# Kernel optimization log

Measured on AMD Instinct MI355X. Metric: run time of the kernel, lower is better.

## Reference

```python
import jax, jax.numpy as jnp
from jax import lax
import numpy as np

# db3 analysis/synthesis filter bank (pywt coefficients)
DEC_LO = np.array([0.035226291882100656, -0.085441273882241486, -0.13501102001039084,
                   0.45987750211933132, 0.80689150931333875, 0.33267055295095688], dtype=np.float32)
DEC_HI = np.array([-0.33267055295095688, 0.80689150931333875, -0.45987750211933132,
                   -0.13501102001039084, 0.085441273882241486, 0.035226291882100656], dtype=np.float32)
REC_LO = DEC_LO[::-1].copy()
REC_HI = np.array([0.035226291882100656, 0.085441273882241486, -0.13501102001039084,
                   -0.45987750211933132, 0.80689150931333875, -0.33267055295095688], dtype=np.float32)
L = 6  # db3 filter length
DN = ('NCHW', 'OIHW', 'NCHW')

# analysis correlation kernels (torch conv2d correlates, pytorch_wavelets pre-flips dec filters)
H0_A = jnp.asarray(DEC_LO[::-1].copy())
H1_A = jnp.asarray(DEC_HI[::-1].copy())
# synthesis: conv_transpose(x, g, stride=2, pad=L-2) == correlate(dilate(x,2), flip(g), pad=1)
G0_S = jnp.asarray(REC_LO[::-1].copy())
G1_S = jnp.asarray(REC_HI[::-1].copy())


def _sep_conv(x, f, axis, stride=1, lhs_dil=1, pad=0):
    """Depthwise 1-D correlation along H (axis=2) or W (axis=3) of an NCHW tensor."""
    C = x.shape[1]
    if axis == 2:
        k = jnp.tile(f.reshape(1, 1, -1, 1), (C, 1, 1, 1))
        strides, dil, padding = (stride, 1), (lhs_dil, 1), ((pad, pad), (0, 0))
    else:
        k = jnp.tile(f.reshape(1, 1, 1, -1), (C, 1, 1, 1))
        strides, dil, padding = (1, stride), (1, lhs_dil), ((0, 0), (pad, pad))
    return lax.conv_general_dilated(x, k, strides, padding, lhs_dilation=dil,
                                    dimension_numbers=DN, feature_group_count=C)


def _dwt2(x):
    # single-level separable 2D DWT, mode='zero' (pytorch_wavelets: rows then cols)
    lo = _sep_conv(x, H0_A, 3, stride=2, pad=L - 2)
    hi = _sep_conv(x, H1_A, 3, stride=2, pad=L - 2)
    ll = _sep_conv(lo, H0_A, 2, stride=2, pad=L - 2)
    lh = _sep_conv(lo, H1_A, 2, stride=2, pad=L - 2)  # yh[:,:,0]
    hl = _sep_conv(hi, H0_A, 2, stride=2, pad=L - 2)  # yh[:,:,1]
    hh = _sep_conv(hi, H1_A, 2, stride=2, pad=L - 2)  # yh[:,:,2]
    return ll, lh, hl, hh


def _idwt2(ll, lh, hl, hh):
    # inverse: cols then rows; transposed conv realized as lhs_dilation=2 + pad 1
    lo = _sep_conv(ll, G0_S, 2, lhs_dil=2, pad=1) + _sep_conv(lh, G1_S, 2, lhs_dil=2, pad=1)
    hi = _sep_conv(hl, G0_S, 2, lhs_dil=2, pad=1) + _sep_conv(hh, G1_S, 2, lhs_dil=2, pad=1)
    return _sep_conv(lo, G0_S, 3, lhs_dil=2, pad=1) + _sep_conv(hi, G1_S, 3, lhs_dil=2, pad=1)


def _dw3x3(x, w):
    # depthwise 3x3, padding 1, no bias; w: (C,1,3,3)
    return lax.conv_general_dilated(x, w, (1, 1), ((1, 1), (1, 1)),
                                    dimension_numbers=DN, feature_group_count=x.shape[1])


def _ssl(x, conv5_w, conv7_w, conv9_w):
    # faithful to original: conv5 applied to BOTH yl and ylh; conv1/conv_cat unused
    ll, lh, hl, hh = _dwt2(x)
    return _idwt2(_dw3x3(ll, conv5_w), _dw3x3(lh, conv5_w),
                  _dw3x3(hl, conv7_w), _dw3x3(hh, conv9_w))


def setup_inputs() -> dict:
    key = jax.random.key(0)
    ks = jax.random.split(key, 7)
    B, C, H, W, HEADS = 4, 256, 192, 192, 8
    s = 0.05
    return {
        'x': jax.random.normal(ks[0], (B, C, H, W), jnp.float32),
        'qkv_w': jax.random.normal(ks[1], (2 * C, C), jnp.float32) * s,        # 1x1 conv C->2C
        'qkv_conv_w': jax.random.normal(ks[2], (2 * C, 1, 3, 3), jnp.float32) * s,  # depthwise 3x3
        'conv5_w': jax.random.normal(ks[3], (C, 1, 3, 3), jnp.float32) * s,
        'conv7_w': jax.random.normal(ks[4], (C, 1, 3, 3), jnp.float32) * s,
        'conv9_w': jax.random.normal(ks[5], (C, 1, 3, 3), jnp.float32) * s,
        'proj_w': jax.random.normal(ks[6], (C, C), jnp.float32) * s,           # 1x1 conv C->C
        'temperature': jnp.ones((1, HEADS, 1, 1), jnp.float32),
        'num_heads': HEADS,
    }


def reference(x, qkv_w, qkv_conv_w, conv5_w, conv7_w, conv9_w, proj_w, temperature, num_heads):
    b, c, h, w = x.shape
    eps = 1e-12
    kv = jnp.einsum('oc,bchw->bohw', qkv_w, x)          # 1x1 conv, no bias
    kv = _dw3x3(kv, qkv_conv_w)
    k, v = jnp.split(kv, 2, axis=1)
    q = _ssl(x, conv5_w, conv7_w, conv9_w)              # wavelet query path, same HxW
    d = c // num_heads
    q = q.reshape(b, num_heads, d, h * w)
    k = k.reshape(b, num_heads, d, h * w)
    v = v.reshape(b, num_heads, d, h * w)
    q = q / jnp.maximum(jnp.linalg.norm(q, axis=-1, keepdims=True), eps)
    k = k / jnp.maximum(jnp.linalg.norm(k, axis=-1, keepdims=True), eps)
    attn = jax.nn.softmax(jnp.einsum('bhdn,bhen->bhde', q, k) * temperature, axis=-1)  # (b,H,d,d)
    out = jnp.einsum('bhde,bhen->bhdn', attn, v).reshape(b, c, h, w)
    return jnp.einsum('oc,bchw->bohw', proj_w, out)
```

## Files before the change

### kernel.cpp

```cpp
#include <hip/hip_runtime.h>
#include <hip/hip_bf16.h>

typedef __hip_bfloat16 bf16;
typedef __attribute__((ext_vector_type(8))) short short8v;
typedef __attribute__((ext_vector_type(4))) float f32x4;

#define NB 4
#define NC 256
#define NPIX 36864
#define NH 192
#define NW 192
#define SW 98
#define SH 98
#define GCH 24

__device__ __constant__ float cH0A[6] = {  0.33267055295095688f,  0.80689150931333875f,  0.45987750211933132f, -0.13501102001039084f, -0.085441273882241486f, 0.035226291882100656f };
__device__ __constant__ float cH1A[6] = {  0.035226291882100656f, 0.085441273882241486f, -0.13501102001039084f, -0.45987750211933132f,  0.80689150931333875f, -0.33267055295095688f };
__device__ __constant__ float cG0S[6] = {  0.035226291882100656f, -0.085441273882241486f, -0.13501102001039084f, 0.45987750211933132f,  0.80689150931333875f,  0.33267055295095688f };
__device__ __constant__ float cG1S[6] = { -0.33267055295095688f,  0.80689150931333875f, -0.45987750211933132f, -0.13501102001039084f,  0.085441273882241486f, 0.035226291882100656f };

__device__ inline unsigned short bfbits(float f) {
    bf16 h = __float2bfloat16(f);
    return *reinterpret_cast<unsigned short*>(&h);
}
__device__ inline float b2f(short s) {
    return __bfloat162float(*reinterpret_cast<const bf16*>(&s));
}

__global__ __launch_bounds__(256) void k_wave(const float* __restrict__ x,
                                              const float* __restrict__ w5, const float* __restrict__ w7,
                                              const float* __restrict__ w9,
                                              bf16* __restrict__ q, float* __restrict__ qsum) {
    int w0 = blockIdx.x * 64, h0 = blockIdx.y * 32;
    int bc = blockIdx.z;
    int c = bc & 255;
    int jh0 = h0 >> 1, jw0 = w0 >> 1;
    int xr0 = h0 - 6;
    int xc0 = w0 - 8;
    __shared__ __align__(16) char smem[40320];
    float (*s_x)[80]   = (float(*)[80])smem;
    float (*s_c)[36]   = (float(*)[36])smem;
    float (*s_lo)[40]  = (float(*)[40])(smem + 14080);
    float (*s_hi)[40]  = (float(*)[40])(smem + 21120);
    float (*s_lh)[36]  = (float(*)[36])(smem + 14080);
    float (*s_sub)[38] = (float(*)[38])(smem + 28160);
    __shared__ float s_w[4][9];
    __shared__ float red[4];
    const float* xp = x + (size_t)bc * NPIX;
    int t = threadIdx.x;
    if (t < 36) {
        int f = t / 9, k = t - f * 9;
        const float* wsel = (f <= 1) ? w5 : (f == 2 ? w7 : w9);
        s_w[f][k] = wsel[c * 9 + k];
    }
    for (int e = t; e < 880; e += 256) {
        int r = e / 20, s = e - r * 20;
        int row = xr0 + r, col0 = xc0 + s * 4;
        float4 v = make_float4(0.f, 0.f, 0.f, 0.f);
        if (row >= 0 && row < NH) {
            if (col0 >= 0 && col0 + 3 < NW) {
                v = *reinterpret_cast<const float4*>(xp + (size_t)row * NW + col0);
            } else {
#pragma unroll
                for (int j = 0; j < 4; ++j) {
                    int cc = col0 + j;
                    if (cc >= 0 && cc < NW) (&v.x)[j] = xp[(size_t)row * NW + cc];
                }
            }
        }
        *reinterpret_cast<float4*>(&s_x[r][s * 4]) = v;
    }
    __syncthreads();
    for (int e = t; e < 836; e += 256) {
        int r = e / 19, g = e - r * 19;
        float v[8];
#pragma unroll
        for (int j = 0; j < 8; ++j) v[j] = s_x[r][4 * g + j];
        float la0 = 0.f, ha0 = 0.f, la1 = 0.f, ha1 = 0.f;
#pragma unroll
        for (int tp = 0; tp < 6; ++tp) {
            la0 = fmaf(v[tp], cH0A[tp], la0);
            ha0 = fmaf(v[tp], cH1A[tp], ha0);
            la1 = fmaf(v[tp + 2], cH0A[tp], la1);
            ha1 = fmaf(v[tp + 2], cH1A[tp], ha1);
        }
        s_lo[r][2 * g] = la0;     s_hi[r][2 * g] = ha0;
        s_lo[r][2 * g + 1] = la1; s_hi[r][2 * g + 1] = ha1;
    }
    __syncthreads();
    for (int e = t; e < 760; e += 256) {
        int r = e / 38, jc = e - r * 38;
        int gr = jh0 - 1 + r, gcol = jw0 - 2 + jc;
        bool inb = (gr >= 0 && gr < SH && gcol >= 0 && gcol < SW);
        float ll = 0.f, lh = 0.f, hl = 0.f, hh = 0.f;
#pragma unroll
        for (int tp = 0; tp < 6; ++tp) {
            float lv = s_lo[2 * r + tp][jc];
            float hv = s_hi[2 * r + tp][jc];
            ll = fmaf(lv, cH0A[tp], ll); lh = fmaf(lv, cH1A[tp], lh);
            hl = fmaf(hv, cH0A[tp], hl); hh = fmaf(hv, cH1A[tp], hh);
        }
        s_sub[r][jc]      = inb ? ll : 0.f;
        s_sub[20 + r][jc] = inb ? lh : 0.f;
        s_sub[40 + r][jc] = inb ? hl : 0.f;
        s_sub[60 + r][jc] = inb ? hh : 0.f;
    }
    __syncthreads();
    for (int e = t; e < 612; e += 256) {
        int pl = e / 153;
        int r2 = e - pl * 153;
        int rp = r2 / 17, gp4 = r2 - rp * 17;
        const float* wp = s_w[pl];
        int rb = pl * 20 + 2 * rp;
        int cc = 2 * gp4;
        float win[4][4];
#pragma unroll
        for (int ri = 0; ri < 4; ++ri)
#pragma unroll
            for (int cj = 0; cj < 4; ++cj)
                win[ri][cj] = s_sub[rb + ri][cc + 1 + cj];
        float wreg[9];
#pragma unroll
        for (int i = 0; i < 9; ++i) wreg[i] = wp[i];
#pragma unroll
        for (int dr = 0; dr < 2; ++dr)
#pragma unroll
            for (int dc = 0; dc < 2; ++dc) {
                float a = 0.f;
#pragma unroll
                for (int ky = 0; ky < 3; ++ky)
#pragma unroll
                    for (int kx = 0; kx < 3; ++kx)
                        a = fmaf(win[dr + ky][dc + kx], wreg[ky * 3 + kx], a);
                s_c[pl * 18 + 2 * rp + dr][cc + dc] = a;
            }
    }
    __syncthreads();
    for (int e = t; e < 1088; e += 256) {
        int row = e / 34, cc = e - row * 34;
        int which = row >> 4, m = row & 15;
        float c0_0 = s_c[which * 36 + m][cc],     c1_0 = s_c[which * 36 + 18 + m][cc];
        float c0_1 = s_c[which * 36 + m + 1][cc], c1_1 = s_c[which * 36 + 18 + m + 1][cc];
        float c0_2 = s_c[which * 36 + m + 2][cc], c1_2 = s_c[which * 36 + 18 + m + 2][cc];
        float ae = c0_0 * cG0S[1] + c0_1 * cG0S[3] + c0_2 * cG0S[5]
                 + c1_0 * cG1S[1] + c1_1 * cG1S[3] + c1_2 * cG1S[5];
        float ao = c0_0 * cG0S[0] + c0_1 * cG0S[2] + c0_2 * cG0S[4]
                 + c1_0 * cG1S[0] + c1_1 * cG1S[2] + c1_2 * cG1S[4];
        s_lh[which * 32 + 2 * m][cc] = ae;
        s_lh[which * 32 + 2 * m + 1][cc] = ao;
    }
    __syncthreads();
    float lsum = 0.f;
    bf16* qp = q + (size_t)bc * NPIX;
#pragma unroll
    for (int it = 0; it < 4; ++it) {
        int e = t + 256 * it;
        int hh = e >> 5, m = e & 31;
        float l0 = s_lh[hh][m],     h0v = s_lh[32 + hh][m];
        float l1 = s_lh[hh][m + 1], h1v = s_lh[32 + hh][m + 1];
        float l2 = s_lh[hh][m + 2], h2v = s_lh[32 + hh][m + 2];
        float ae = l0 * cG0S[1] + l1 * cG0S[3] + l2 * cG0S[5]
                 + h0v * cG1S[1] + h1v * cG1S[3] + h2v * cG1S[5];
        float ao = l0 * cG0S[0] + l1 * cG0S[2] + l2 * cG0S[4]
                 + h0v * cG1S[0] + h1v * cG1S[2] + h2v * cG1S[4];
        unsigned pack = (unsigned)bfbits(ae) | ((unsigned)bfbits(ao) << 16);
        *reinterpret_cast<unsigned*>(qp + (size_t)(h0 + hh) * NW + w0 + 2 * m) = pack;
        lsum = fmaf(ae, ae, lsum);
        lsum = fmaf(ao, ao, lsum);
    }
#pragma unroll
    for (int off = 32; off; off >>= 1) lsum += __shfl_down(lsum, off, 64);
    if ((t & 63) == 0) red[t >> 6] = lsum;
    __syncthreads();
    if (t == 0) atomicAdd(&qsum[bc], red[0] + red[1] + red[2] + red[3]);
}

__global__ __launch_bounds__(256) void k_cvtw(const float* __restrict__ w, bf16* __restrict__ wb) {
    int idx = blockIdx.x * 256 + threadIdx.x;
    if (idx < 512 * 256) wb[idx] = __float2bfloat16(w[idx]);
}

__global__ __launch_bounds__(512) void k_gemm_x(const float* __restrict__ x, const bf16* __restrict__ Wbf,
                                                bf16* __restrict__ Out) {
    __shared__ __align__(16) short As[256 * 64];
    __shared__ __align__(16) short Bs[128 * 64];
    int nt = blockIdx.x, b = blockIdx.y;
    int n0 = nt * 128;
    const float* xb = x + (size_t)b * NC * NPIX;
    int t = threadIdx.x;
    int wv = t >> 6, l = t & 63;
    int wo = wv >> 1, wn = wv & 1;
    int lrow = l >> 3, cbs0 = l & 7;
    int nq = t & 31;
    int cg = t >> 5;
    int c0 = cg * 4;
    f32x4 z4 = {0.f, 0.f, 0.f, 0.f};
    f32x4 acc[4][4];
#pragma unroll
    for (int m = 0; m < 4; ++m)
#pragma unroll
        for (int nf = 0; nf < 4; ++nf) acc[m][nf] = z4;
    for (int kc = 0; kc < 256; kc += 64) {
        __syncthreads();
#pragma unroll
        for (int i = 0; i < 4; ++i) {
            int r0 = wv * 32 + i * 8;
            int r = r0 + lrow;
            int cb = cbs0 ^ (r & 7);
            __builtin_amdgcn_global_load_lds(
                (const __attribute__((address_space(1))) void*)(Wbf + (size_t)r * NC + kc + cb * 8),
                (__attribute__((address_space(3))) void*)(As + r0 * 64), 16, 0, 0);
        }
        float4 xv[4];
#pragma unroll
        for (int ci = 0; ci < 4; ++ci)
            xv[ci] = *reinterpret_cast<const float4*>(xb + (size_t)(kc + c0 + ci) * NPIX + n0 + nq * 4);
#pragma unroll
        for (int j = 0; j < 4; ++j) {
            int n = nq * 4 + j;
            ushort4 u;
            u.x = bfbits((&xv[0].x)[j]); u.y = bfbits((&xv[1].x)[j]);
            u.z = bfbits((&xv[2].x)[j]); u.w = bfbits((&xv[3].x)[j]);
            int unit = (c0 >> 3) ^ (n & 7);
            int half = (c0 >> 2) & 1;
            *reinterpret_cast<ushort4*>(Bs + n * 64 + unit * 8 + half * 4) = u;
        }
        __syncthreads();
#pragma unroll
        for (int kk = 0; kk < 2; ++kk) {
            int col8 = kk * 4 + (l >> 4);
            short8v av[4], bv[4];
#pragma unroll
            for (int m = 0; m < 4; ++m) {
                int row = wo * 64 + m * 16 + (l & 15);
                av[m] = *(const short8v*)(As + row * 64 + (col8 ^ (row & 7)) * 8);
            }
#pragma unroll
            for (int nf = 0; nf < 4; ++nf) {
                int row = wn * 64 + nf * 16 + (l & 15);
                bv[nf] = *(const short8v*)(Bs + row * 64 + (col8 ^ (row & 7)) * 8);
            }
#pragma unroll
            for (int m = 0; m < 4; ++m)
#pragma unroll
                for (int nf = 0; nf < 4; ++nf)
                    acc[m][nf] = __builtin_amdgcn_mfma_f32_16x16x32_bf16(av[m], bv[nf], acc[m][nf], 0, 0, 0);
        }
    }
    bf16* ob = Out + (size_t)b * NC * NPIX;
#pragma unroll
    for (int m = 0; m < 4; ++m)
#pragma unroll
        for (int nf = 0; nf < 4; ++nf)
#pragma unroll
            for (int r = 0; r < 4; ++r) {
                int oo = wo * 64 + m * 16 + (l >> 4) * 4 + r;
                int nn = n0 + wn * 64 + nf * 16 + (l & 15);
                ob[(size_t)oo * NPIX + nn] = __float2bfloat16(acc[m][nf][r]);
            }
}

template <typename TOUT>
__global__ __launch_bounds__(256) void k_gemm_bf(const bf16* __restrict__ X, const bf16* __restrict__ Wm,
                                                 int wStride, TOUT* __restrict__ Out) {
    __shared__ __align__(16) short As[128 * 64];
    __shared__ __align__(16) short Bs[128 * 64];
    int nt = blockIdx.x, ot = blockIdx.y, b = blockIdx.z;
    int n0 = nt * 128, o0 = ot * 128;
    const bf16* xb = X + (size_t)b * NPIX * NC;
    const bf16* Wb = Wm + (size_t)b * wStride;
    int t = threadIdx.x;
    int wv = t >> 6, l = t & 63;
    int wr = wv >> 1, wc = wv & 1;
    int lrow = l >> 3, cbs0 = l & 7;
    f32x4 z4 = {0.f, 0.f, 0.f, 0.f};
    f32x4 acc[4][4];
#pragma unroll
    for (int m = 0; m < 4; ++m)
#pragma unroll
        for (int nf = 0; nf < 4; ++nf) acc[m][nf] = z4;
    for (int kc = 0; kc < 256; kc += 64) {
        __syncthreads();
#pragma unroll
        for (int i = 0; i < 4; ++i) {
            int r0 = wv * 32 + i * 8;
            int r = r0 + lrow;
            int cb = cbs0 ^ (r & 7);
            __builtin_amdgcn_global_load_lds(
                (const __attribute__((address_space(1))) void*)(Wb + (size_t)(o0 + r) * NC + kc + cb * 8),
                (__attribute__((address_space(3))) void*)(As + r0 * 64), 16, 0, 0);
            __builtin_amdgcn_global_load_lds(
                (const __attribute__((address_space(1))) void*)(xb + (size_t)(n0 + r) * NC + kc + cb * 8),
                (__attribute__((address_space(3))) void*)(Bs + r0 * 64), 16, 0, 0);
        }
        __syncthreads();
#pragma unroll
        for (int kk = 0; kk < 2; ++kk) {
            int col8 = kk * 4 + (l >> 4);
            short8v av[4], bv[4];
#pragma unroll
            for (int m = 0; m < 4; ++m) {
                int row = wr * 64 + m * 16 + (l & 15);
                av[m] = *(const short8v*)(As + row * 64 + (col8 ^ (row & 7)) * 8);
            }
#pragma unroll
            for (int nf = 0; nf < 4; ++nf) {
                int row = wc * 64 + nf * 16 + (l & 15);
                bv[nf] = *(const short8v*)(Bs + row * 64 + (col8 ^ (row & 7)) * 8);
            }
#pragma unroll
            for (int m = 0; m < 4; ++m)
#pragma unroll
                for (int nf = 0; nf < 4; ++nf)
                    acc[m][nf] = __builtin_amdgcn_mfma_f32_16x16x32_bf16(av[m], bv[nf], acc[m][nf], 0, 0, 0);
        }
    }
    TOUT* ob = Out + (size_t)b * NC * NPIX;
#pragma unroll
    for (int m = 0; m < 4; ++m)
#pragma unroll
        for (int nf = 0; nf < 4; ++nf)
#pragma unroll
            for (int r = 0; r < 4; ++r) {
                int oo = o0 + wr * 64 + m * 16 + (l >> 4) * 4 + r;
                int nn = n0 + wc * 64 + nf * 16 + (l & 15);
                if constexpr (sizeof(TOUT) == 2)
                    ob[(size_t)oo * NPIX + nn] = __float2bfloat16(acc[m][nf][r]);
                else
                    ob[(size_t)oo * NPIX + nn] = acc[m][nf][r];
            }
}

__device__ inline short8v dw8(const bf16* __restrict__ chan, int r, int cb,
                              const float* __restrict__ w, float& ks) {
    float v[3][10];
#pragma unroll
    for (int ri = 0; ri < 3; ++ri) {
        int r2 = r + ri - 1;
        if (r2 < 0 || r2 >= NH) {
#pragma unroll
            for (int j = 0; j < 10; ++j) v[ri][j] = 0.f;
        } else {
            const bf16* p = chan + (size_t)r2 * NW + cb;
            short8v m = *(const short8v*)p;
            v[ri][0] = (cb > 0) ? __bfloat162float(p[-1]) : 0.f;
#pragma unroll
            for (int j = 0; j < 8; ++j) v[ri][j + 1] = b2f(m[j]);
            v[ri][9] = (cb < 184) ? __bfloat162float(p[8]) : 0.f;
        }
    }
    short8v out;
#pragma unroll
    for (int j = 0; j < 8; ++j) {
        float a = 0.f;
#pragma unroll
        for (int ri = 0; ri < 3; ++ri) {
            a = fmaf(v[ri][j],     w[ri * 3 + 0], a);
            a = fmaf(v[ri][j + 1], w[ri * 3 + 1], a);
            a = fmaf(v[ri][j + 2], w[ri * 3 + 2], a);
        }
        ks = fmaf(a, a, ks);
        out[j] = (short)bfbits(a);
    }
    return out;
}

__global__ __launch_bounds__(256) void k_gram_dw(const bf16* __restrict__ qbf, const bf16* __restrict__ kraw,
                                                 const float* __restrict__ dwW,
                                                 float* __restrict__ gpart, float* __restrict__ ksum) {
    int chunk = blockIdx.x;
    int bh = blockIdx.y; int b = bh >> 3, h = bh & 7;
    const bf16* qb = qbf + ((size_t)b * NC + h * 32) * NPIX;
    const bf16* kb = kraw + ((size_t)b * NC + h * 32) * NPIX;
    __shared__ float sg[4][1024];
    __shared__ float ksh[32];
    int t = threadIdx.x;
    int wv = t >> 6, l = t & 63;
    int dlo = l & 15, kslot = l >> 4;
    float wA[9], wB[9];
#pragma unroll
    for (int i = 0; i < 9; ++i) {
        wA[i] = dwW[(h * 32 + dlo) * 9 + i];
        wB[i] = dwW[(h * 32 + dlo + 16) * 9 + i];
    }
    const bf16* q0 = qb + (size_t)dlo * NPIX;
    const bf16* q1 = qb + (size_t)(dlo + 16) * NPIX;
    const bf16* k0 = kb + (size_t)dlo * NPIX;
    const bf16* k1 = kb + (size_t)(dlo + 16) * NPIX;
    f32x4 z4 = {0.f, 0.f, 0.f, 0.f};
    f32x4 a00 = z4, a01 = z4, a10 = z4, a11 = z4;
    float ks0 = 0.f, ks1 = 0.f;
    int r0 = chunk * 8 + wv * 2;
#pragma unroll
    for (int rr = 0; rr < 2; ++rr) {
        int r = r0 + rr;
#pragma unroll
        for (int c0 = 0; c0 < 192; c0 += 32) {
            int cb = c0 + kslot * 8;
            short8v av0 = *(const short8v*)(q0 + (size_t)r * NW + cb);
            short8v av1 = *(const short8v*)(q1 + (size_t)r * NW + cb);
            short8v bv0 = dw8(k0, r, cb, wA, ks0);
            short8v bv1 = dw8(k1, r, cb, wB, ks1);
            a00 = __builtin_amdgcn_mfma_f32_16x16x32_bf16(av0, bv0, a00, 0, 0, 0);
            a01 = __builtin_amdgcn_mfma_f32_16x16x32_bf16(av0, bv1, a01, 0, 0, 0);
            a10 = __builtin_amdgcn_mfma_f32_16x16x32_bf16(av1, bv0, a10, 0, 0, 0);
            a11 = __builtin_amdgcn_mfma_f32_16x16x32_bf16(av1, bv1, a11, 0, 0, 0);
        }
    }
    if (t < 32) ksh[t] = 0.f;
#pragma unroll
    for (int j = 0; j < 4; ++j) {
        int dA = kslot * 4 + j, dB = 16 + kslot * 4 + j;
        sg[wv][dA * 32 + dlo]      = a00[j];
        sg[wv][dA * 32 + 16 + dlo] = a01[j];
        sg[wv][dB * 32 + dlo]      = a10[j];
        sg[wv][dB * 32 + 16 + dlo] = a11[j];
    }
    __syncthreads();
    float* gp = gpart + ((size_t)bh * GCH + chunk) * 1024;
#pragma unroll
    for (int i = 0; i < 4; ++i) {
        int e = t + 256 * i;
        gp[e] = sg[0][e] + sg[1][e] + sg[2][e] + sg[3][e];
    }
    atomicAdd(&ksh[dlo], ks0);
    atomicAdd(&ksh[dlo + 16], ks1);
    __syncthreads();
    if (t < 32) atomicAdd(&ksum[b * NC + h * 32 + t], ksh[t]);
}

__global__ __launch_bounds__(1024) void k_attn(const float* __restrict__ gpart, const float* __restrict__ qsum,
                                               const float* __restrict__ ksum, const float* __restrict__ temp,
                                               float* __restrict__ attn) {
    int bh = blockIdx.x;
    int b = bh >> 3, h = bh & 7;
    int t = threadIdx.x;
    int d = t >> 5, e = t & 31;
    float s = 0.f;
    for (int i = 0; i < GCH; ++i) s += gpart[((size_t)bh * GCH + i) * 1024 + t];
    float rq = 1.f / fmaxf(sqrtf(qsum[b * NC + h * 32 + d]), 1e-12f);
    float rk = 1.f / fmaxf(sqrtf(ksum[b * NC + h * 32 + e]), 1e-12f);
    s *= rq * rk * temp[h];
    float m = s;
#pragma unroll
    for (int off = 16; off; off >>= 1) m = fmaxf(m, __shfl_xor(m, off, 32));
    float ex = expf(s - m);
    float sum = ex;
#pragma unroll
    for (int off = 16; off; off >>= 1) sum += __shfl_xor(sum, off, 32);
    attn[(size_t)bh * 1024 + t] = ex / sum;
}

__global__ __launch_bounds__(256) void k_wfold(const float* __restrict__ proj, const float* __restrict__ attn,
                                               bf16* __restrict__ wfbf) {
    int o = blockIdx.x, b = blockIdx.y;
    int t = threadIdx.x;
    int h = t >> 5, e = t & 31;
    const float* ap = attn + (size_t)(b * 8 + h) * 1024 + e;
    const float* pp = proj + o * NC + h * 32;
    float acc = 0.f;
#pragma unroll
    for (int d = 0; d < 32; ++d) acc = fmaf(pp[d], ap[d * 32], acc);
    wfbf[((size_t)b * NC + o) * NC + t] = __float2bfloat16(acc);
}

__global__ __launch_bounds__(256) void k_dwv(const bf16* __restrict__ vraw, const float* __restrict__ dwW,
                                             bf16* __restrict__ v2T) {
    int r = blockIdx.x;
    int cg = blockIdx.y;
    int b = blockIdx.z;
    __shared__ short s_v[3][32][204];
    const bf16* vb = vraw + ((size_t)b * NC + cg * 32) * NPIX;
    int t = threadIdx.x;
    for (int idx = t; idx < 4800; idx += 256) {
        int ri = idx / 1600;
        int rem = idx - ri * 1600;
        int e = rem / 50, j = rem - e * 50;
        int gr = r + ri - 1;
        int gc0 = -4 + 4 * j;
        ushort4 u = make_ushort4(0, 0, 0, 0);
        if (gr >= 0 && gr < NH && gc0 >= 0 && gc0 + 3 < NW)
            u = *reinterpret_cast<const ushort4*>(vb + (size_t)e * NPIX + (size_t)gr * NW + gc0);
        *reinterpret_cast<ushort4*>(&s_v[ri][e][4 * j]) = u;
    }
    int e = t & 31;
    int wslot = t >> 5;
    float w9[9];
#pragma unroll
    for (int i = 0; i < 9; ++i) w9[i] = dwW[(256 + cg * 32 + e) * 9 + i];
    __syncthreads();
    bf16* ob = v2T + ((size_t)b * NPIX + (size_t)r * NW) * NC + cg * 32 + e;
#pragma unroll
    for (int wi = 0; wi < 24; ++wi) {
        int w = wslot + 8 * wi;
        int cbase = w + 3;
        float a = 0.f;
#pragma unroll
        for (int ri = 0; ri < 3; ++ri) {
            a = fmaf(b2f(s_v[ri][e][cbase]),     w9[ri * 3 + 0], a);
            a = fmaf(b2f(s_v[ri][e][cbase + 1]), w9[ri * 3 + 1], a);
            a = fmaf(b2f(s_v[ri][e][cbase + 2]), w9[ri * 3 + 2], a);
        }
        ob[(size_t)w * NC] = __float2bfloat16(a);
    }
}


extern "C" void kernel_launch(void* const* d_in, const int* in_sizes, int n_in,
                              void* d_out, int out_size, void* d_ws, size_t ws_size,
                              hipStream_t stream) {
    (void)in_sizes; (void)n_in; (void)out_size;
    const float* x      = (const float*)d_in[0];
    const float* qkv_w  = (const float*)d_in[1];
    const float* qkv_cw = (const float*)d_in[2];
    const float* w5     = (const float*)d_in[3];
    const float* w7     = (const float*)d_in[4];
    const float* w9     = (const float*)d_in[5];
    const float* projw  = (const float*)d_in[6];
    const float* temp   = (const float*)d_in[7];

    const size_t OFF_SM    = 78675968;
    const size_t OFF_WBF   = OFF_SM;
    const size_t OFF_QSUM  = OFF_SM + 262144;
    const size_t OFF_KSUM  = OFF_QSUM + 4096;
    const size_t OFF_GPART = OFF_KSUM + 4096;
    const size_t OFF_ATTN  = OFF_GPART + 3145728;
    const size_t OFF_WF    = OFF_ATTN + 131072;
    const size_t WS_NEED   = OFF_WF + 524288;
    if (ws_size < WS_NEED) return;

    char* ws = (char*)d_ws;
    bf16*  kraw  = (bf16*)ws;
    bf16*  v2T   = (bf16*)ws;
    bf16*  wbf   = (bf16*)(ws + OFF_WBF);
    float* qsum  = (float*)(ws + OFF_QSUM);
    float* ksum  = (float*)(ws + OFF_KSUM);
    float* gpart = (float*)(ws + OFF_GPART);
    float* attn  = (float*)(ws + OFF_ATTN);
    bf16*  wfbf  = (bf16*)(ws + OFF_WF);

    bf16*  qbf  = (bf16*)((char*)d_out + 75497472);
    bf16*  vraw = (bf16*)((char*)d_out + 75497472);
    float* out  = (float*)d_out;

    hipMemsetAsync(ws + OFF_QSUM, 0, 8192, stream);

    k_wave<<<dim3(3, 6, NB * NC), 256, 0, stream>>>(x, w5, w7, w9, qbf, qsum);

    k_cvtw<<<512, 256, 0, stream>>>(qkv_w, wbf);

    k_gemm_x<<<dim3(288, NB), 512, 0, stream>>>(x, wbf, kraw);
    k_gram_dw<<<dim3(GCH, 32), 256, 0, stream>>>(qbf, kraw, qkv_cw, gpart, ksum);

    k_attn<<<32, 1024, 0, stream>>>(gpart, qsum, ksum, temp, attn);
    k_wfold<<<dim3(256, NB), 256, 0, stream>>>(projw, attn, wfbf);

    k_gemm_x<<<dim3(288, NB), 512, 0, stream>>>(x, wbf + 256 * 256, vraw);
    k_dwv<<<dim3(NH, 8, NB), 256, 0, stream>>>(vraw, qkv_cw, v2T);
    k_gemm_bf<float><<<dim3(288, 2, NB), 256, 0, stream>>>(v2T, wfbf, 65536, out);
}
```

Measured before the change: 520.1 us.

## Fuse K and V projection GEMMs to share one pass over x

Merges the two separate 1x1-conv GEMM launches for K and V into one kernel. It loads and converts each fp32 x tile to bf16 once, then runs MFMA against both weight halves, reloading only the weight tile in LDS between them. This removes a second full read and conversion of the large fp32 input. The cost is a doubled accumulator register footprint and extra barriers per K-chunk. V output is relocated to the start of the output buffer so it does not overlap q. The wavelet kernel's LDS reads and writes are also vectorized to float4/float2.

```diff
diff --git a/kernel.cpp b/kernel.cpp
--- a/kernel.cpp
+++ b/kernel.cpp
@@ -73,9 +73,9 @@
     __syncthreads();
     for (int e = t; e < 836; e += 256) {
         int r = e / 19, g = e - r * 19;
-        float v[8];
-#pragma unroll
-        for (int j = 0; j < 8; ++j) v[j] = s_x[r][4 * g + j];
+        float4 va = *reinterpret_cast<const float4*>(&s_x[r][4 * g]);
+        float4 vb = *reinterpret_cast<const float4*>(&s_x[r][4 * g + 4]);
+        float v[8] = { va.x, va.y, va.z, va.w, vb.x, vb.y, vb.z, vb.w };
         float la0 = 0.f, ha0 = 0.f, la1 = 0.f, ha1 = 0.f;
 #pragma unroll
         for (int tp = 0; tp < 6; ++tp) {
@@ -84,8 +84,8 @@
             la1 = fmaf(v[tp + 2], cH0A[tp], la1);
             ha1 = fmaf(v[tp + 2], cH1A[tp], ha1);
         }
-        s_lo[r][2 * g] = la0;     s_hi[r][2 * g] = ha0;
-        s_lo[r][2 * g + 1] = la1; s_hi[r][2 * g + 1] = ha1;
+        *reinterpret_cast<float2*>(&s_lo[r][2 * g]) = make_float2(la0, la1);
+        *reinterpret_cast<float2*>(&s_hi[r][2 * g]) = make_float2(ha0, ha1);
     }
     __syncthreads();
     for (int e = t; e < 760; e += 256) {
@@ -180,8 +180,8 @@
     if (idx < 512 * 256) wb[idx] = __float2bfloat16(w[idx]);
 }
 
-__global__ __launch_bounds__(512) void k_gemm_x(const float* __restrict__ x, const bf16* __restrict__ Wbf,
-                                                bf16* __restrict__ Out) {
+__global__ __launch_bounds__(512) void k_gemm_kv(const float* __restrict__ x, const bf16* __restrict__ Wbf,
+                                                 bf16* __restrict__ kout, bf16* __restrict__ vout) {
     __shared__ __align__(16) short As[256 * 64];
     __shared__ __align__(16) short Bs[128 * 64];
     int nt = blockIdx.x, b = blockIdx.y;
@@ -195,11 +195,11 @@
     int cg = t >> 5;
     int c0 = cg * 4;
     f32x4 z4 = {0.f, 0.f, 0.f, 0.f};
-    f32x4 acc[4][4];
+    f32x4 acc_k[4][4], acc_v[4][4];
 #pragma unroll
     for (int m = 0; m < 4; ++m)
 #pragma unroll
-        for (int nf = 0; nf < 4; ++nf) acc[m][nf] = z4;
+        for (int nf = 0; nf < 4; ++nf) { acc_k[m][nf] = z4; acc_v[m][nf] = z4; }
     for (int kc = 0; kc < 256; kc += 64) {
         __syncthreads();
 #pragma unroll
@@ -211,19 +211,21 @@
                 (const __attribute__((address_space(1))) void*)(Wbf + (size_t)r * NC + kc + cb * 8),
                 (__attribute__((address_space(3))) void*)(As + r0 * 64), 16, 0, 0);
         }
-        float4 xv[4];
-#pragma unroll
-        for (int ci = 0; ci < 4; ++ci)
-            xv[ci] = *reinterpret_cast<const float4*>(xb + (size_t)(kc + c0 + ci) * NPIX + n0 + nq * 4);
-#pragma unroll
-        for (int j = 0; j < 4; ++j) {
-            int n = nq * 4 + j;
-            ushort4 u;
-            u.x = bfbits((&xv[0].x)[j]); u.y = bfbits((&xv[1].x)[j]);
-            u.z = bfbits((&xv[2].x)[j]); u.w = bfbits((&xv[3].x)[j]);
-            int unit = (c0 >> 3) ^ (n & 7);
-            int half = (c0 >> 2) & 1;
-            *reinterpret_cast<ushort4*>(Bs + n * 64 + unit * 8 + half * 4) = u;
+        {
+            float4 xv[4];
+#pragma unroll
+            for (int ci = 0; ci < 4; ++ci)
+                xv[ci] = *reinterpret_cast<const float4*>(xb + (size_t)(kc + c0 + ci) * NPIX + n0 + nq * 4);
+#pragma unroll
+            for (int j = 0; j < 4; ++j) {
+                int n = nq * 4 + j;
+                ushort4 u;
+                u.x = bfbits((&xv[0].x)[j]); u.y = bfbits((&xv[1].x)[j]);
+                u.z = bfbits((&xv[2].x)[j]); u.w = bfbits((&xv[3].x)[j]);
+                int unit = (c0 >> 3) ^ (n & 7);
+                int half = (c0 >> 2) & 1;
+                *reinterpret_cast<ushort4*>(Bs + n * 64 + unit * 8 + half * 4) = u;
+            }
         }
         __syncthreads();
 #pragma unroll
@@ -244,10 +246,42 @@
             for (int m = 0; m < 4; ++m)
 #pragma unroll
                 for (int nf = 0; nf < 4; ++nf)
-                    acc[m][nf] = __builtin_amdgcn_mfma_f32_16x16x32_bf16(av[m], bv[nf], acc[m][nf], 0, 0, 0);
-        }
-    }
-    bf16* ob = Out + (size_t)b * NC * NPIX;
+                    acc_k[m][nf] = __builtin_amdgcn_mfma_f32_16x16x32_bf16(av[m], bv[nf], acc_k[m][nf], 0, 0, 0);
+        }
+        __syncthreads();
+#pragma unroll
+        for (int i = 0; i < 4; ++i) {
+            int r0 = wv * 32 + i * 8;
+            int r = r0 + lrow;
+            int cb = cbs0 ^ (r & 7);
+            __builtin_amdgcn_global_load_lds(
+                (const __attribute__((address_space(1))) void*)(Wbf + 65536 + (size_t)r * NC + kc + cb * 8),
+                (__attribute__((address_space(3))) void*)(As + r0 * 64), 16, 0, 0);
+        }
+        __syncthreads();
+#pragma unroll
+        for (int kk = 0; kk < 2; ++kk) {
+            int col8 = kk * 4 + (l >> 4);
+            short8v av[4], bv[4];
+#pragma unroll
+            for (int m = 0; m < 4; ++m) {
+                int row = wo * 64 + m * 16 + (l & 15);
+                av[m] = *(const short8v*)(As + row * 64 + (col8 ^ (row & 7)) * 8);
+            }
+#pragma unroll
+            for (int nf = 0; nf < 4; ++nf) {
+                int row = wn * 64 + nf * 16 + (l & 15);
+                bv[nf] = *(const short8v*)(Bs + row * 64 + (col8 ^ (row & 7)) * 8);
+            }
+#pragma unroll
+            for (int m = 0; m < 4; ++m)
+#pragma unroll
+                for (int nf = 0; nf < 4; ++nf)
+                    acc_v[m][nf] = __builtin_amdgcn_mfma_f32_16x16x32_bf16(av[m], bv[nf], acc_v[m][nf], 0, 0, 0);
+        }
+    }
+    bf16* okb = kout + (size_t)b * NC * NPIX;
+    bf16* ovb = vout + (size_t)b * NC * NPIX;
 #pragma unroll
     for (int m = 0; m < 4; ++m)
 #pragma unroll
@@ -256,7 +290,8 @@
             for (int r = 0; r < 4; ++r) {
                 int oo = wo * 64 + m * 16 + (l >> 4) * 4 + r;
                 int nn = n0 + wn * 64 + nf * 16 + (l & 15);
-                ob[(size_t)oo * NPIX + nn] = __float2bfloat16(acc[m][nf][r]);
+                okb[(size_t)oo * NPIX + nn] = __float2bfloat16(acc_k[m][nf][r]);
+                ovb[(size_t)oo * NPIX + nn] = __float2bfloat16(acc_v[m][nf][r]);
             }
 }
 
@@ -539,8 +574,8 @@
     float* attn  = (float*)(ws + OFF_ATTN);
     bf16*  wfbf  = (bf16*)(ws + OFF_WF);
 
+    bf16*  vraw = (bf16*)d_out;
     bf16*  qbf  = (bf16*)((char*)d_out + 75497472);
-    bf16*  vraw = (bf16*)((char*)d_out + 75497472);
     float* out  = (float*)d_out;
 
     hipMemsetAsync(ws + OFF_QSUM, 0, 8192, stream);
@@ -549,13 +584,12 @@
 
     k_cvtw<<<512, 256, 0, stream>>>(qkv_w, wbf);
 
-    k_gemm_x<<<dim3(288, NB), 512, 0, stream>>>(x, wbf, kraw);
+    k_gemm_kv<<<dim3(288, NB), 512, 0, stream>>>(x, wbf, kraw, vraw);
+
     k_gram_dw<<<dim3(GCH, 32), 256, 0, stream>>>(qbf, kraw, qkv_cw, gpart, ksum);
-
     k_attn<<<32, 1024, 0, stream>>>(gpart, qsum, ksum, temp, attn);
     k_wfold<<<dim3(256, NB), 256, 0, stream>>>(projw, attn, wfbf);
 
-    k_gemm_x<<<dim3(288, NB), 512, 0, stream>>>(x, wbf + 256 * 256, vraw);
     k_dwv<<<dim3(NH, 8, NB), 256, 0, stream>>>(vraw, qkv_cw, v2T);
     k_gemm_bf<float><<<dim3(288, 2, NB), 256, 0, stream>>>(v2T, wfbf, 65536, out);
 }
```

Measured after the change: 526.1 us. No clear change (+1.2%).
